# Optimization experiments

Hardware: AMD Instinct MI355X
Metric: run time of the kernel (lower is better)

The kernel has to match this reference:

```python
import jax, jax.numpy as jnp
import numpy as np

KERNEL_NUM = 32
SUPPORT_NUM = 4


def setup_inputs() -> dict:
    key = jax.random.key(0)
    k1, k2, k3, k4 = jax.random.split(key, 4)
    bs, v, n = 4, 8192, 20
    stdv = 1.0 / np.sqrt(SUPPORT_NUM * KERNEL_NUM)
    vertices = jax.random.normal(k1, (bs, v, 3), dtype=jnp.float32)
    neighbor_index = jax.random.randint(k2, (bs, v, n), 0, v)
    weights = jax.random.uniform(k3, (1, 1, SUPPORT_NUM, KERNEL_NUM), minval=-stdv, maxval=stdv, dtype=jnp.float32)
    displacement = jax.random.uniform(k4, (3, SUPPORT_NUM * KERNEL_NUM), minval=-stdv, maxval=stdv, dtype=jnp.float32)
    return {"neighbor_index": neighbor_index, "vertices": vertices,
            "weights": weights, "displacement": displacement}


def reference(neighbor_index, vertices, weights, displacement):
    bs, v, n = neighbor_index.shape
    # gather neighbors per batch: (bs, v, n, 3)
    neighbors = jax.vmap(lambda verts, idx: verts[idx])(vertices, neighbor_index)
    disp = neighbors - vertices[:, :, None, :]                      # (bs, v, n, 3)
    theta = jnp.einsum('bvnd,dk->bvnk', disp, displacement)          # (bs, v, n, S*K)
    theta = jax.nn.relu(theta)
    theta = theta.reshape(bs, v, n, SUPPORT_NUM, KERNEL_NUM)
    theta = jnp.max(theta, axis=2) * weights                         # (bs, v, S, K)
    feature = jnp.sum(theta, axis=2)                                 # (bs, v, K)
    return feature
```

## Files before the change

### kernel.cpp

```cpp
#include <hip/hip_runtime.h>

#define BS 4
#define NV 8192
#define NN 20
#define SN 4
#define KN 32
#define GPB 8
#define BLOCK (GPB * KN)

__global__ __launch_bounds__(BLOCK) void op3d_kernel(
    const int*   __restrict__ nbr,
    const float* __restrict__ verts,
    const float* __restrict__ wgt,
    const float* __restrict__ disp,
    float*       __restrict__ out)
{
    __shared__ float4 sdx[GPB * NN];

    const int tx  = threadIdx.x;
    const int bv0 = blockIdx.x * GPB;

    const int k = tx & (KN - 1);
    float D0[SN], D1[SN], D2[SN], w[SN];
#pragma unroll
    for (int s = 0; s < SN; ++s) {
        const int col = s * KN + k;
        D0[s] = disp[0 * SN * KN + col];
        D1[s] = disp[1 * SN * KN + col];
        D2[s] = disp[2 * SN * KN + col];
        w[s]  = wgt[col];
    }

    if (tx < GPB * NN) {
        const int bv  = bv0 + tx / NN;
        const int b   = bv >> 13;
        const int idx = nbr[bv0 * NN + tx];
        const float* vb = verts + (size_t)b * NV * 3;
        const float nx = vb[idx * 3 + 0];
        const float ny = vb[idx * 3 + 1];
        const float nz = vb[idx * 3 + 2];
        const float vx = verts[(size_t)bv * 3 + 0];
        const float vy = verts[(size_t)bv * 3 + 1];
        const float vz = verts[(size_t)bv * 3 + 2];
        sdx[tx] = make_float4(nx - vx, ny - vy, nz - vz, 0.f);
    }
    __syncthreads();

    const int g = tx >> 5;
    const float4* sg = &sdx[g * NN];
    float m[SN] = {0.f, 0.f, 0.f, 0.f};
#pragma unroll
    for (int j = 0; j < NN; ++j) {
        const float4 d = sg[j];
#pragma unroll
        for (int s = 0; s < SN; ++s) {
            float t = fmaf(d.x, D0[s], fmaf(d.y, D1[s], d.z * D2[s]));
            m[s] = fmaxf(m[s], fmaxf(t, 0.f));
        }
    }

    float acc = 0.f;
#pragma unroll
    for (int s = 0; s < SN; ++s) acc = fmaf(m[s], w[s], acc);

    out[(size_t)(bv0 + g) * KN + k] = acc;
}

extern "C" void kernel_launch(void* const* d_in, const int* in_sizes, int n_in,
                              void* d_out, int out_size, void* d_ws, size_t ws_size,
                              hipStream_t stream) {
    const int*   nbr   = (const int*)d_in[0];
    const float* verts = (const float*)d_in[1];
    const float* wgt   = (const float*)d_in[2];
    const float* disp  = (const float*)d_in[3];
    float* out = (float*)d_out;

    const int grid = (BS * NV) / GPB;
    op3d_kernel<<<grid, BLOCK, 0, stream>>>(nbr, verts, wgt, disp, out);
}
```

Before: 69.17 us.

## Double-buffer neighbor gathers across two vertex batches and compute two kernels per thread

Each block now handles two batches of 16 vertices. The gathers for the second batch are issued into registers before the first batch is computed, then written to a second shared-memory buffer, so global gather latency can overlap with compute. Each thread now computes two kernel outputs using float2 loads and stores, and the shared-memory rows are padded. The relu is folded into the zero-initialised max. The trade-off is four times fewer blocks and higher register use per thread, which may reduce how much latency the GPU can hide through parallelism.

```diff
diff --git a/kernel.cpp b/kernel.cpp
--- a/kernel.cpp
+++ b/kernel.cpp
@@ -5,65 +5,124 @@
 #define NN 20
 #define SN 4
 #define KN 32
-#define GPB 8
-#define BLOCK (GPB * KN)
 
-__global__ __launch_bounds__(BLOCK) void op3d_kernel(
+#define KPT 2
+#define TPG (KN / KPT)
+#define GP  16
+#define BLOCK (GP * TPG)
+#define NB 2
+#define SLOTS (GP * NN)
+#define LDP (NN + 1)
+
+__global__ __launch_bounds__(BLOCK, 4) void op3d_kernel(
     const int*   __restrict__ nbr,
     const float* __restrict__ verts,
     const float* __restrict__ wgt,
     const float* __restrict__ disp,
     float*       __restrict__ out)
 {
-    __shared__ float4 sdx[GPB * NN];
+    __shared__ float4 sdx[NB][GP * LDP];
 
-    const int tx  = threadIdx.x;
-    const int bv0 = blockIdx.x * GPB;
+    const int tx     = threadIdx.x;
+    const int batchA = blockIdx.x * NB;
+    const int batchB = batchA + 1;
 
-    const int k = tx & (KN - 1);
-    float D0[SN], D1[SN], D2[SN], w[SN];
+    const int  i0   = tx;
+    const int  i1   = tx + BLOCK;
+    const bool has1 = (i1 < SLOTS);
+    const int idxA0 = nbr[(size_t)batchA * SLOTS + i0];
+    const int idxB0 = nbr[(size_t)batchB * SLOTS + i0];
+    int idxA1 = 0, idxB1 = 0;
+    if (has1) {
+        idxA1 = nbr[(size_t)batchA * SLOTS + i1];
+        idxB1 = nbr[(size_t)batchB * SLOTS + i1];
+    }
+
+    const int kk = (tx & (TPG - 1)) * KPT;
+    const int g  = tx / TPG;
+    float2 D0[SN], D1[SN], D2[SN], w[SN];
 #pragma unroll
     for (int s = 0; s < SN; ++s) {
-        const int col = s * KN + k;
-        D0[s] = disp[0 * SN * KN + col];
-        D1[s] = disp[1 * SN * KN + col];
-        D2[s] = disp[2 * SN * KN + col];
-        w[s]  = wgt[col];
+        const int col = s * KN + kk;
+        D0[s] = *(const float2*)(disp + 0 * SN * KN + col);
+        D1[s] = *(const float2*)(disp + 1 * SN * KN + col);
+        D2[s] = *(const float2*)(disp + 2 * SN * KN + col);
+        w[s]  = *(const float2*)(wgt  + col);
     }
 
-    if (tx < GPB * NN) {
-        const int bv  = bv0 + tx / NN;
-        const int b   = bv >> 13;
-        const int idx = nbr[bv0 * NN + tx];
-        const float* vb = verts + (size_t)b * NV * 3;
-        const float nx = vb[idx * 3 + 0];
-        const float ny = vb[idx * 3 + 1];
-        const float nz = vb[idx * 3 + 2];
-        const float vx = verts[(size_t)bv * 3 + 0];
-        const float vy = verts[(size_t)bv * 3 + 1];
-        const float vz = verts[(size_t)bv * 3 + 2];
-        sdx[tx] = make_float4(nx - vx, ny - vy, nz - vz, 0.f);
+    const int gi0 = i0 / NN, j0 = i0 - gi0 * NN;
+    const int gi1 = i1 / NN, j1 = i1 - gi1 * NN;
+
+    {
+        const int bv = batchA * GP + gi0;
+        const float* np = verts + ((size_t)(bv & ~(NV - 1)) + idxA0) * 3;
+        const float* vp = verts + (size_t)bv * 3;
+        const float4 d = make_float4(np[0] - vp[0], np[1] - vp[1], np[2] - vp[2], 0.f);
+        float4 d1 = make_float4(0.f, 0.f, 0.f, 0.f);
+        if (has1) {
+            const int bv1 = batchA * GP + gi1;
+            const float* np1 = verts + ((size_t)(bv1 & ~(NV - 1)) + idxA1) * 3;
+            const float* vp1 = verts + (size_t)bv1 * 3;
+            d1 = make_float4(np1[0] - vp1[0], np1[1] - vp1[1], np1[2] - vp1[2], 0.f);
+        }
+        sdx[0][gi0 * LDP + j0] = d;
+        if (has1) sdx[0][gi1 * LDP + j1] = d1;
     }
     __syncthreads();
 
-    const int g = tx >> 5;
-    const float4* sg = &sdx[g * NN];
-    float m[SN] = {0.f, 0.f, 0.f, 0.f};
+    float nx0, ny0, nz0, vx0, vy0, vz0;
+    {
+        const int bv = batchB * GP + gi0;
+        const float* np = verts + ((size_t)(bv & ~(NV - 1)) + idxB0) * 3;
+        const float* vp = verts + (size_t)bv * 3;
+        nx0 = np[0]; ny0 = np[1]; nz0 = np[2];
+        vx0 = vp[0]; vy0 = vp[1]; vz0 = vp[2];
+    }
+    float nx1 = 0.f, ny1 = 0.f, nz1 = 0.f, vx1 = 0.f, vy1 = 0.f, vz1 = 0.f;
+    if (has1) {
+        const int bv = batchB * GP + gi1;
+        const float* np = verts + ((size_t)(bv & ~(NV - 1)) + idxB1) * 3;
+        const float* vp = verts + (size_t)bv * 3;
+        nx1 = np[0]; ny1 = np[1]; nz1 = np[2];
+        vx1 = vp[0]; vy1 = vp[1]; vz1 = vp[2];
+    }
+
+    auto compute_store = [&](int buf, int batch) {
+        const float4* sg = &sdx[buf][g * LDP];
+        float2 m[SN];
 #pragma unroll
-    for (int j = 0; j < NN; ++j) {
-        const float4 d = sg[j];
+        for (int s = 0; s < SN; ++s) m[s] = make_float2(0.f, 0.f);
+#pragma unroll
+        for (int jp = 0; jp < NN / 2; ++jp) {
+            const float4 da = sg[2 * jp];
+            const float4 db = sg[2 * jp + 1];
+#pragma unroll
+            for (int s = 0; s < SN; ++s) {
+                const float ta0 = fmaf(da.x, D0[s].x, fmaf(da.y, D1[s].x, da.z * D2[s].x));
+                const float tb0 = fmaf(db.x, D0[s].x, fmaf(db.y, D1[s].x, db.z * D2[s].x));
+                const float ta1 = fmaf(da.x, D0[s].y, fmaf(da.y, D1[s].y, da.z * D2[s].y));
+                const float tb1 = fmaf(db.x, D0[s].y, fmaf(db.y, D1[s].y, db.z * D2[s].y));
+                m[s].x = fmaxf(m[s].x, fmaxf(ta0, tb0));
+                m[s].y = fmaxf(m[s].y, fmaxf(ta1, tb1));
+            }
+        }
+        float accx = 0.f, accy = 0.f;
 #pragma unroll
         for (int s = 0; s < SN; ++s) {
-            float t = fmaf(d.x, D0[s], fmaf(d.y, D1[s], d.z * D2[s]));
-            m[s] = fmaxf(m[s], fmaxf(t, 0.f));
+            accx = fmaf(m[s].x, w[s].x, accx);
+            accy = fmaf(m[s].y, w[s].y, accy);
         }
-    }
+        const int bv = batch * GP + g;
+        *(float2*)(out + (size_t)bv * KN + kk) = make_float2(accx, accy);
+    };
 
-    float acc = 0.f;
-#pragma unroll
-    for (int s = 0; s < SN; ++s) acc = fmaf(m[s], w[s], acc);
+    compute_store(0, batchA);
 
-    out[(size_t)(bv0 + g) * KN + k] = acc;
+    sdx[1][gi0 * LDP + j0] = make_float4(nx0 - vx0, ny0 - vy0, nz0 - vz0, 0.f);
+    if (has1) sdx[1][gi1 * LDP + j1] = make_float4(nx1 - vx1, ny1 - vy1, nz1 - vz1, 0.f);
+    __syncthreads();
+
+    compute_store(1, batchB);
 }
 
 extern "C" void kernel_launch(void* const* d_in, const int* in_sizes, int n_in,
@@ -75,6 +134,6 @@
     const float* disp  = (const float*)d_in[3];
     float* out = (float*)d_out;
 
-    const int grid = (BS * NV) / GPB;
+    const int grid = (BS * NV) / (GP * NB);
     op3d_kernel<<<grid, BLOCK, 0, stream>>>(nbr, verts, wgt, disp, out);
 }
```

Result: no change. 69.12 us (-0.1%).
